# Optimization experiments

Hardware: AMD Instinct MI355X
Metric: run time of the kernel (lower is better)

The kernel has to match this reference:

```python
import jax, jax.numpy as jnp
import numpy as np

H, D_MODEL, D_AUX, D_POS = 8, 512, 256, 128
D_K, D_A, D_P = D_MODEL // H, D_AUX // H, D_POS // H  # 64, 32, 16
M1, M2, T, B = 8, 8, 1024, 8
EPS = 1e-12


def _l2norm(x):
    # F.normalize(x, p=2, dim=-1)
    return x / jnp.maximum(jnp.linalg.norm(x, axis=-1, keepdims=True), EPS)


def _tn_transform(S):
    # S: [B,H,T,T] pairwise <Q_t, K_s>. tn[a,b] = mean over diagonal window
    # t in [-min(M1,min(a,b)), min(M2,T-1-max(a,b))] of S[a+t, b+t].
    num = jnp.zeros_like(S)
    for t in range(-M1, M2 + 1):  # small fixed window (17 offsets)
        lo, hi = max(0, -t), T - max(0, t)
        num = num.at[..., lo:hi, lo:hi].add(S[..., lo + t:hi + t, lo + t:hi + t])
    idx = jnp.arange(T)
    mn = jnp.minimum(idx[:, None], idx[None, :])
    mx = jnp.maximum(idx[:, None], idx[None, :])
    cnt = (jnp.minimum(M1, mn) + jnp.minimum(M2, T - 1 - mx) + 1).astype(S.dtype)
    return num / cnt


def _forward(x, aux, pos, Wq, bq, Wk, bk, Wv, bv, Wqa, bqa, Wka, bka, Wqp, bqp, Wkp, bkp, WO, bO, w, wa, wp, graph_dep):
    g = graph_dep.astype(x.dtype)           # [D_K, D_K] binary dependency mask
    m_node = jnp.tile(g, (1, H))            # per-head SparseLinear mask [D_K, D_MODEL]
    m_out = jnp.tile(g, (H, H))             # W_O mask: graph_dependency.repeat(h, h)
    Q = _l2norm(jnp.einsum('btm,hkm->bhtk', x, Wq * m_node) + bq[None, :, None, :])
    K = _l2norm(jnp.einsum('btm,hkm->bhtk', x, Wk * m_node) + bk[None, :, None, :])
    V = jnp.einsum('btm,hkm->bhtk', x, Wv * m_node) + bv[None, :, None, :]
    tn = _tn_transform(jnp.einsum('bhtk,bhsk->bhts', Q, K))
    QA = _l2norm(jnp.einsum('bta,hca->bhtc', aux, Wqa) + bqa[None, :, None, :])
    KA = _l2norm(jnp.einsum('bta,hca->bhtc', aux, Wka) + bka[None, :, None, :])
    QP = _l2norm(jnp.einsum('btp,hcp->bhtc', pos, Wqp) + bqp[None, :, None, :])
    KP = _l2norm(jnp.einsum('btp,hcp->bhtc', pos, Wkp) + bkp[None, :, None, :])
    sim = (w[0, 0] * tn
           + wa[0, 0] * jnp.einsum('bhtc,bhsc->bhts', QA, KA)
           + wp[0, 0] * jnp.einsum('bhtc,bhsc->bhts', QP, KP))
    attn = jax.nn.softmax(sim, axis=-1)     # [B,H,T,T]
    deta = jnp.einsum('bhts,bhsk->bhtk', attn, V).transpose(0, 2, 1, 3).reshape(B, T, D_MODEL)
    out = x + jnp.einsum('btd,ed->bte', deta, WO * m_out) + bO
    attn_matrix = attn.transpose(0, 2, 1, 3).reshape(B, T, H * T)
    return out, attn_matrix, deta


def setup_inputs() -> dict:
    key = jax.random.key(0)
    ks = jax.random.split(key, 16)
    sc = 0.05
    f32 = jnp.float32
    return {
        'x': jax.random.normal(ks[0], (B, T, D_MODEL), f32),
        'aux': jax.random.normal(ks[1], (B, T, D_AUX), f32),
        'pos': jax.random.normal(ks[2], (B, T, D_POS), f32),
        'Wq': jax.random.normal(ks[3], (H, D_K, D_MODEL), f32) * sc,
        'bq': jnp.zeros((H, D_K), f32),
        'Wk': jax.random.normal(ks[4], (H, D_K, D_MODEL), f32) * sc,
        'bk': jnp.zeros((H, D_K), f32),
        'Wv': jax.random.normal(ks[5], (H, D_K, D_MODEL), f32) * sc,
        'bv': jnp.zeros((H, D_K), f32),
        'Wqa': jax.random.normal(ks[6], (H, D_A, D_AUX), f32) * sc,
        'bqa': jnp.zeros((H, D_A), f32),
        'Wka': jax.random.normal(ks[7], (H, D_A, D_AUX), f32) * sc,
        'bka': jnp.zeros((H, D_A), f32),
        'Wqp': jax.random.normal(ks[8], (H, D_P, D_POS), f32) * sc,
        'bqp': jnp.zeros((H, D_P), f32),
        'Wkp': jax.random.normal(ks[9], (H, D_P, D_POS), f32) * sc,
        'bkp': jnp.zeros((H, D_P), f32),
        'WO': jax.random.normal(ks[10], (D_MODEL, D_MODEL), f32) * sc,
        'bO': jnp.zeros((D_MODEL,), f32),
        'w': jax.random.normal(ks[11], (1, 1), f32),
        'wa': jax.random.normal(ks[12], (1, 1), f32),
        'wp': jax.random.normal(ks[13], (1, 1), f32),
        'graph_dep': jax.random.randint(ks[14], (D_K, D_K), 0, 2, jnp.int32),
    }


def reference(x, aux, pos, Wq, bq, Wk, bk, Wv, bv, Wqa, bqa, Wka, bka, Wqp, bqp, Wkp, bkp, WO, bO, w, wa, wp, graph_dep):
    return _forward(x, aux, pos, Wq, bq, Wk, bk, Wv, bv, Wqa, bqa, Wka, bka, Wqp, bqp, Wkp, bkp, WO, bO, w, wa, wp, graph_dep)
```

## Files before the change

### kernel.cpp

```cpp
#include <hip/hip_runtime.h>
#include <math.h>

#define NB 8
#define NH 8
#define NT 1024
#define DMODEL 512

typedef short bh8 __attribute__((ext_vector_type(8)));
typedef float fx4 __attribute__((ext_vector_type(4)));

__device__ __forceinline__ unsigned short f2bf(float f) {
  union { float f; unsigned int u; } v; v.f = f;
  unsigned int u = v.u + 0x7FFFu + ((v.u >> 16) & 1u);
  return (unsigned short)(u >> 16);
}
__device__ __forceinline__ float bf2f(unsigned short h) {
  union { unsigned int u; float f; } v; v.u = ((unsigned int)h) << 16;
  return v.f;
}

__global__ __launch_bounds__(256) void k_prep(
    const float* __restrict__ Wq, const float* __restrict__ Wk,
    const float* __restrict__ Wv, const float* __restrict__ WO,
    const int* __restrict__ g,
    const float* __restrict__ Wqa, const float* __restrict__ Wka,
    const float* __restrict__ Wqp, const float* __restrict__ Wkp,
    unsigned short* __restrict__ Wqkvcm, unsigned short* __restrict__ WO_mb,
    unsigned short* __restrict__ Wacm, unsigned short* __restrict__ Wpcm,
    unsigned short* __restrict__ qcf, unsigned short* __restrict__ kcf)
{
  int stride = gridDim.x * 256;
  int tid0 = blockIdx.x * 256 + threadIdx.x;
  for (int i = tid0; i < 1536 * 512; i += stride) {
    int m = i & 511;
    int j = i >> 9;
    int k = j & 63;
    int hh = (j >> 6) & 7;
    int qkv = j >> 9;
    const float* W = (qkv == 0) ? Wq : (qkv == 1 ? Wk : Wv);
    float val = W[(hh * 64 + k) * 512 + m] * (float)g[k * 64 + (m & 63)];
    Wqkvcm[((size_t)(m >> 3) * 1536 + j) * 8 + (m & 7)] = f2bf(val);
  }
  for (int i = tid0; i < 512 * 512; i += stride) {
    int d = i & 511, e = i >> 9;
    WO_mb[i] = f2bf(WO[i] * (float)g[(e & 63) * 64 + (d & 63)]);
  }
  for (int i = tid0; i < 512 * 256; i += stride) {
    int a = i & 255, j = i >> 8;
    float val = (j < 256) ? Wqa[j * 256 + a] : Wka[(j - 256) * 256 + a];
    Wacm[((size_t)(a >> 3) * 512 + j) * 8 + (a & 7)] = f2bf(val);
  }
  for (int i = tid0; i < 256 * 128; i += stride) {
    int p = i & 127, j = i >> 7;
    float val = (j < 128) ? Wqp[j * 128 + p] : Wkp[(j - 128) * 128 + p];
    Wpcm[((size_t)(p >> 3) * 256 + j) * 8 + (p & 7)] = f2bf(val);
  }
  for (int i = tid0; i < 64 * 16384; i += stride) {
    int bh = i >> 14, rest = i & 16383;
    size_t addr = (size_t)(bh * 8 + 6) * 8192 + rest;
    qcf[addr] = 0; kcf[addr] = 0;
  }
}

__global__ __launch_bounds__(256) void k_tocm(
    const float* __restrict__ src, unsigned short* __restrict__ dst, int M, int K)
{
  __shared__ unsigned short t16[64][80];
  const int bm = blockIdx.x * 64, bk = blockIdx.y * 64;
  const int tid = threadIdx.x;
  {
    int r = tid >> 2, q = tid & 3;
    const float* sp = src + (size_t)(bm + r) * K + bk + q * 16;
#pragma unroll
    for (int j = 0; j < 4; ++j) {
      float4 v = *(const float4*)(sp + j * 4);
      t16[r][q * 16 + j * 4 + 0] = f2bf(v.x);
      t16[r][q * 16 + j * 4 + 1] = f2bf(v.y);
      t16[r][q * 16 + j * 4 + 2] = f2bf(v.z);
      t16[r][q * 16 + j * 4 + 3] = f2bf(v.w);
    }
  }
  __syncthreads();
  {
    int cq = tid >> 5, rr = tid & 31;
#pragma unroll
    for (int h = 0; h < 2; ++h) {
      int r2 = rr + h * 32;
      unsigned short* dp = dst + ((size_t)((bk >> 3) + cq) * M + bm + r2) * 8;
      *(int4*)dp = *(const int4*)&t16[r2][cq * 8];
    }
  }
}

__global__ __launch_bounds__(256) void k_gqkv(
    const unsigned short* __restrict__ Acm, const unsigned short* __restrict__ Bcm,
    const float* __restrict__ bq, const float* __restrict__ bk, const float* __restrict__ bv,
    const float* __restrict__ w,
    unsigned short* __restrict__ Qf, unsigned short* __restrict__ Kf,
    unsigned short* __restrict__ Vrow)
{
  const int M = 8192, N = 1536, K = 512;
  const int bm = blockIdx.y * 128, bn = blockIdx.x * 128;
  const int tid = threadIdx.x, lane = tid & 63, wv = tid >> 6;
  const int wr = wv >> 1, wc = wv & 1;
  const int lrow = lane & 15, lgrp = lane >> 4;
  fx4 acc[4][4];
#pragma unroll
  for (int m = 0; m < 4; ++m)
#pragma unroll
    for (int n = 0; n < 4; ++n) acc[m][n] = (fx4){0.f, 0.f, 0.f, 0.f};
  for (int k0 = 0; k0 < K; k0 += 32) {
    bh8 af[4], bf[4];
#pragma unroll
    for (int m = 0; m < 4; ++m)
      af[m] = *(const bh8*)(Acm + (((size_t)((k0 >> 3) + lgrp)) * M + bm + wr * 64 + m * 16 + lrow) * 8);
#pragma unroll
    for (int n = 0; n < 4; ++n)
      bf[n] = *(const bh8*)(Bcm + (((size_t)((k0 >> 3) + lgrp)) * N + bn + wc * 64 + n * 16 + lrow) * 8);
#pragma unroll
    for (int m = 0; m < 4; ++m)
#pragma unroll
      for (int n = 0; n < 4; ++n)
        acc[m][n] = __builtin_amdgcn_mfma_f32_16x16x32_bf16(af[m], bf[n], acc[m][n], 0, 0, 0);
  }
  const int qkv = bn >> 9;
  const int hh = ((bn + wc * 64) >> 6) & 7;
  const float w0 = w[0];
  const float* bias = (qkv == 0) ? bq : (qkv == 1 ? bk : bv);
  float bvals[4];
#pragma unroll
  for (int n = 0; n < 4; ++n) bvals[n] = bias[hh * 64 + n * 16 + lrow];
#pragma unroll
  for (int m = 0; m < 4; ++m)
#pragma unroll
    for (int r = 0; r < 4; ++r) {
      int row = bm + wr * 64 + m * 16 + lgrp * 4 + r;
      int b = row >> 10, t = row & 1023;
      int bh = b * 8 + hh;
      float v0 = acc[m][0][r] + bvals[0];
      float v1 = acc[m][1][r] + bvals[1];
      float v2 = acc[m][2][r] + bvals[2];
      float v3 = acc[m][3][r] + bvals[3];
      if (qkv < 2) {
        float p = v0 * v0 + v1 * v1 + v2 * v2 + v3 * v3;
        p += __shfl_xor(p, 1); p += __shfl_xor(p, 2);
        p += __shfl_xor(p, 4); p += __shfl_xor(p, 8);
        float rn = 1.0f / fmaxf(sqrtf(p), 1e-12f);
        if (qkv == 0) rn *= w0;
        unsigned short* dst = (qkv == 0) ? Qf : Kf;
        size_t base = (size_t)bh * 65536 + (size_t)(lrow >> 3) * 8192 + (size_t)t * 8 + (lrow & 7);
        dst[base + 0 * 16384] = f2bf(v0 * rn);
        dst[base + 1 * 16384] = f2bf(v1 * rn);
        dst[base + 2 * 16384] = f2bf(v2 * rn);
        dst[base + 3 * 16384] = f2bf(v3 * rn);
      } else {
        size_t vb = ((size_t)bh * NT + t) * 64 + lrow;
        Vrow[vb + 0]  = f2bf(v0);
        Vrow[vb + 16] = f2bf(v1);
        Vrow[vb + 32] = f2bf(v2);
        Vrow[vb + 48] = f2bf(v3);
      }
    }
}

__global__ __launch_bounds__(256) void k_gaux(
    const unsigned short* __restrict__ Acm, const unsigned short* __restrict__ Bcm,
    const float* __restrict__ bqa, const float* __restrict__ bka,
    const float* __restrict__ wa,
    unsigned short* __restrict__ qcf, unsigned short* __restrict__ kcf)
{
  const int M = 8192, N = 512, K = 256;
  const int bm = blockIdx.y * 128, bn = blockIdx.x * 128;
  const int tid = threadIdx.x, lane = tid & 63, wv = tid >> 6;
  const int wr = wv >> 1, wc = wv & 1;
  const int lrow = lane & 15, lgrp = lane >> 4;
  fx4 acc[4][4];
#pragma unroll
  for (int m = 0; m < 4; ++m)
#pragma unroll
    for (int n = 0; n < 4; ++n) acc[m][n] = (fx4){0.f, 0.f, 0.f, 0.f};
  for (int k0 = 0; k0 < K; k0 += 32) {
    bh8 af[4], bf[4];
#pragma unroll
    for (int m = 0; m < 4; ++m)
      af[m] = *(const bh8*)(Acm + (((size_t)((k0 >> 3) + lgrp)) * M + bm + wr * 64 + m * 16 + lrow) * 8);
#pragma unroll
    for (int n = 0; n < 4; ++n)
      bf[n] = *(const bh8*)(Bcm + (((size_t)((k0 >> 3) + lgrp)) * N + bn + wc * 64 + n * 16 + lrow) * 8);
#pragma unroll
    for (int m = 0; m < 4; ++m)
#pragma unroll
      for (int n = 0; n < 4; ++n)
        acc[m][n] = __builtin_amdgcn_mfma_f32_16x16x32_bf16(af[m], bf[n], acc[m][n], 0, 0, 0);
  }
  const int isK = (bn >> 8) & 1;
  const int hh0 = (((bn & 255) + wc * 64) >> 5) & 7;
  const float wa0 = wa[0];
  const float* bias = isK ? bka : bqa;
  float bvals[4];
#pragma unroll
  for (int n = 0; n < 4; ++n) bvals[n] = bias[(hh0 + (n >> 1)) * 32 + (n & 1) * 16 + lrow];
  unsigned short* dst = isK ? kcf : qcf;
  const float scale = isK ? 1.0f : wa0;
#pragma unroll
  for (int m = 0; m < 4; ++m)
#pragma unroll
    for (int r = 0; r < 4; ++r) {
      int row = bm + wr * 64 + m * 16 + lgrp * 4 + r;
      int b = row >> 10, t = row & 1023;
      float v0 = acc[m][0][r] + bvals[0];
      float v1 = acc[m][1][r] + bvals[1];
      float v2 = acc[m][2][r] + bvals[2];
      float v3 = acc[m][3][r] + bvals[3];
      float plo = v0 * v0 + v1 * v1;
      float phi = v2 * v2 + v3 * v3;
      plo += __shfl_xor(plo, 1); plo += __shfl_xor(plo, 2);
      plo += __shfl_xor(plo, 4); plo += __shfl_xor(plo, 8);
      phi += __shfl_xor(phi, 1); phi += __shfl_xor(phi, 2);
      phi += __shfl_xor(phi, 4); phi += __shfl_xor(phi, 8);
      float rlo = scale / fmaxf(sqrtf(plo), 1e-12f);
      float rhi = scale / fmaxf(sqrtf(phi), 1e-12f);
      size_t b0 = (size_t)(b * 8 + hh0) * 65536 + (size_t)(lrow >> 3) * 8192 + (size_t)t * 8 + (lrow & 7);
      size_t b1 = (size_t)(b * 8 + hh0 + 1) * 65536 + (size_t)(lrow >> 3) * 8192 + (size_t)t * 8 + (lrow & 7);
      dst[b0 + 0]     = f2bf(v0 * rlo);
      dst[b0 + 16384] = f2bf(v1 * rlo);
      dst[b1 + 0]     = f2bf(v2 * rhi);
      dst[b1 + 16384] = f2bf(v3 * rhi);
    }
}

__global__ __launch_bounds__(256) void k_gpos(
    const unsigned short* __restrict__ Acm, const unsigned short* __restrict__ Bcm,
    const float* __restrict__ bqp, const float* __restrict__ bkp,
    const float* __restrict__ wp,
    unsigned short* __restrict__ qcf, unsigned short* __restrict__ kcf)
{
  const int M = 8192, N = 256, K = 128;
  const int bm = blockIdx.y * 128, bn = blockIdx.x * 128;
  const int tid = threadIdx.x, lane = tid & 63, wv = tid >> 6;
  const int wr = wv >> 1, wc = wv & 1;
  const int lrow = lane & 15, lgrp = lane >> 4;
  fx4 acc[4][4];
#pragma unroll
  for (int m = 0; m < 4; ++m)
#pragma unroll
    for (int n = 0; n < 4; ++n) acc[m][n] = (fx4){0.f, 0.f, 0.f, 0.f};
  for (int k0 = 0; k0 < K; k0 += 32) {
    bh8 af[4], bf[4];
#pragma unroll
    for (int m = 0; m < 4; ++m)
      af[m] = *(const bh8*)(Acm + (((size_t)((k0 >> 3) + lgrp)) * M + bm + wr * 64 + m * 16 + lrow) * 8);
#pragma unroll
    for (int n = 0; n < 4; ++n)
      bf[n] = *(const bh8*)(Bcm + (((size_t)((k0 >> 3) + lgrp)) * N + bn + wc * 64 + n * 16 + lrow) * 8);
#pragma unroll
    for (int m = 0; m < 4; ++m)
#pragma unroll
      for (int n = 0; n < 4; ++n)
        acc[m][n] = __builtin_amdgcn_mfma_f32_16x16x32_bf16(af[m], bf[n], acc[m][n], 0, 0, 0);
  }
  const int isK = (bn >> 7) & 1;
  const int bh0 = (((bn & 127) + wc * 64) >> 4) & 7;
  const float wp0 = wp[0];
  const float* bias = isK ? bkp : bqp;
  float bvals[4];
#pragma unroll
  for (int n = 0; n < 4; ++n) bvals[n] = bias[(bh0 + n) * 16 + lrow];
  unsigned short* dst = isK ? kcf : qcf;
  const float scale = isK ? 1.0f : wp0;
#pragma unroll
  for (int m = 0; m < 4; ++m)
#pragma unroll
    for (int r = 0; r < 4; ++r) {
      int row = bm + wr * 64 + m * 16 + lgrp * 4 + r;
      int b = row >> 10, t = row & 1023;
      float v[4];
      v[0] = acc[m][0][r] + bvals[0];
      v[1] = acc[m][1][r] + bvals[1];
      v[2] = acc[m][2][r] + bvals[2];
      v[3] = acc[m][3][r] + bvals[3];
#pragma unroll
      for (int n = 0; n < 4; ++n) {
        float p = v[n] * v[n];
        p += __shfl_xor(p, 1); p += __shfl_xor(p, 2);
        p += __shfl_xor(p, 4); p += __shfl_xor(p, 8);
        float rn = scale / fmaxf(sqrtf(p), 1e-12f);
        size_t addr = (size_t)(b * 8 + bh0 + n) * 65536 + (size_t)(4 + (lrow >> 3)) * 8192
                    + (size_t)t * 8 + (lrow & 7);
        dst[addr] = f2bf(v[n] * rn);
      }
    }
}

__global__ __launch_bounds__(256) void k_vtr(
    const unsigned short* __restrict__ Vrow, unsigned short* __restrict__ Vc)
{
  __shared__ unsigned short tile[64][72];
  const int tt = blockIdx.x, bh = blockIdx.y;
  const int tid = threadIdx.x;
  const int r = tid & 63, g = tid >> 6;
  const unsigned short* src = Vrow + ((size_t)bh * NT + tt * 64 + r) * 64 + g * 16;
  int4 v0 = *(const int4*)(src);
  int4 v1 = *(const int4*)(src + 8);
  const unsigned short* pv0 = (const unsigned short*)&v0;
  const unsigned short* pv1 = (const unsigned short*)&v1;
#pragma unroll
  for (int j = 0; j < 8; ++j) tile[g * 16 + j][r] = pv0[j];
#pragma unroll
  for (int j = 0; j < 8; ++j) tile[g * 16 + 8 + j][r] = pv1[j];
  __syncthreads();
  unsigned short* dst0 = Vc + ((size_t)(bh * 128 + tt * 8 + g * 2) * 64 + r) * 8;
  unsigned short* dst1 = Vc + ((size_t)(bh * 128 + tt * 8 + g * 2 + 1) * 64 + r) * 8;
  *(int4*)dst0 = *(const int4*)&tile[r][g * 16];
  *(int4*)dst1 = *(const int4*)&tile[r][g * 16 + 8];
}

__global__ __launch_bounds__(256) void k_sim(
    const unsigned short* __restrict__ Qf, const unsigned short* __restrict__ Kf,
    const unsigned short* __restrict__ qcf, const unsigned short* __restrict__ kcf,
    float* __restrict__ lsumP, float* __restrict__ attn)
{
  __shared__ float Se[80][81];
  __shared__ unsigned short Pd[64][66];
  const int flat = blockIdx.x;
  const int wgid = (flat & 7) * 512 + (flat >> 3);
  const int bh = wgid >> 6;
  const int ctg = (wgid >> 4) & 3;
  const int at = wgid & 15;
  const int a0 = at * 64;
  const int b = bh >> 3, hh = bh & 7;
  const int tid = threadIdx.x;
  const int lane = tid & 63, wv = tid >> 6;
  const int lrow16 = lane & 15, lgrp = lane >> 4;
  const bh8 zfrag = {0, 0, 0, 0, 0, 0, 0, 0};
  const int base_cl = (wv * 16 + lane) & 63;
  float lacc[16];
#pragma unroll
  for (int s = 0; s < 16; ++s) lacc[s] = 0.f;

  const unsigned short* Qc = Qf + (size_t)(bh * 8 + lgrp) * NT * 8;
  const unsigned short* Kc = Kf + (size_t)(bh * 8 + lgrp) * NT * 8;

  bh8 qa0, qa1;
  {
    const unsigned short* qb = qcf + ((size_t)(bh * 8 + lgrp) * NT + a0 + wv * 16 + lrow16) * 8;
    qa0 = *(const bh8*)(qb);
    qa1 = *(const bh8*)(qb + (size_t)4 * NT * 8);
  }

  for (int ct = ctg * 4; ct < ctg * 4 + 4; ++ct) {
    const int c0 = ct * 64;
    __syncthreads();

#pragma unroll
    for (int i = 0; i < 7; ++i) {
      int tt = wv + 4 * i;
      if (tt < 25) {
        int tr = tt / 5, tc = tt % 5;
        int ar = a0 - 8 + tr * 16 + lrow16;
        int kr = c0 - 8 + tc * 16 + lrow16;
        bool av = (unsigned)ar < (unsigned)NT;
        bool bv = (unsigned)kr < (unsigned)NT;
        const unsigned short* ap = Qc + (size_t)(av ? ar : 0) * 8;
        const unsigned short* bp = Kc + (size_t)(bv ? kr : 0) * 8;
        bh8 af0 = av ? *(const bh8*)(ap) : zfrag;
        bh8 af1 = av ? *(const bh8*)(ap + (size_t)4 * NT * 8) : zfrag;
        bh8 bf0 = bv ? *(const bh8*)(bp) : zfrag;
        bh8 bf1 = bv ? *(const bh8*)(bp + (size_t)4 * NT * 8) : zfrag;
        fx4 acc = {0.f, 0.f, 0.f, 0.f};
        acc = __builtin_amdgcn_mfma_f32_16x16x32_bf16(af0, bf0, acc, 0, 0, 0);
        acc = __builtin_amdgcn_mfma_f32_16x16x32_bf16(af1, bf1, acc, 0, 0, 0);
#pragma unroll
        for (int r = 0; r < 4; ++r)
          Se[tr * 16 + lgrp * 4 + r][tc * 16 + lrow16] = acc[r];
      }
    }

#pragma unroll
    for (int n = 0; n < 4; ++n) {
      const unsigned short* kb = kcf + ((size_t)(bh * 8 + lgrp) * NT + c0 + n * 16 + lrow16) * 8;
      bh8 kb0 = *(const bh8*)(kb);
      bh8 kb1 = *(const bh8*)(kb + (size_t)4 * NT * 8);
      fx4 pacc = {0.f, 0.f, 0.f, 0.f};
      pacc = __builtin_amdgcn_mfma_f32_16x16x32_bf16(qa0, kb0, pacc, 0, 0, 0);
      pacc = __builtin_amdgcn_mfma_f32_16x16x32_bf16(qa1, kb1, pacc, 0, 0, 0);
#pragma unroll
      for (int r = 0; r < 4; ++r)
        Pd[wv * 16 + lgrp * 4 + r][n * 16 + lrow16] = f2bf(pacc[r]);
    }

    __syncthreads();

    float dval = 0.f;
    {
      int rr = wv * 16 + lrow16;
#pragma unroll
      for (int u = 0; u <= 16; ++u) dval += Se[rr + u][u];
    }

    float num = 0.f;
#pragma unroll
    for (int s = 0; s < 16; ++s) {
      int a_l = wv * 16 + s;
      int c_l = (base_cl + s) & 63;
      if (s == 0) {
        num = 0.f;
#pragma unroll
        for (int u = 0; u <= 16; ++u) num += Se[a_l + u][c_l + u];
      } else {
        int cm1 = (c_l == 0) ? 0 : (c_l - 1);
        float up = Se[a_l + 16][c_l + 16] - Se[a_l - 1][cm1];
        float dS = __shfl(dval, s);
        num = (c_l == 0) ? dS : (num + up);
      }
      int a = a0 + a_l, c = c0 + c_l;
      int mn = min(a, c), mx = max(a, c);
      float cntf = (float)(min(8, mn) + min(8, 1023 - mx) + 1);
      float sim = num * __builtin_amdgcn_rcpf(cntf) + bf2f(Pd[a_l][c_l]);
      float pe = __expf(sim);
      lacc[s] += pe;
      attn[(((size_t)(b * NT + a)) * NH + hh) * NT + c] = pe;
    }
  }

#pragma unroll
  for (int s = 0; s < 16; ++s) {
    float v = lacc[s];
#pragma unroll
    for (int off = 32; off; off >>= 1) v += __shfl_xor(v, off);
    if (lane == 0)
      lsumP[(size_t)ctg * 65536 + (size_t)bh * NT + a0 + wv * 16 + s] = v;
  }
}

__global__ __launch_bounds__(256) void k_pv(
    const unsigned short* __restrict__ Vc, const float* __restrict__ lsumP,
    float* __restrict__ attn, float* __restrict__ deta,
    unsigned short* __restrict__ detab)
{
  const int at = blockIdx.x, bh = blockIdx.y;
  const int a0 = at * 64;
  const int b = bh >> 3, hh = bh & 7;
  const int tid = threadIdx.x, lane = tid & 63, wv = tid >> 6;
  const int lrow = lane & 15, lgrp = lane >> 4;
  const int arow = a0 + wv * 16 + lrow;
  const size_t lidx = (size_t)bh * NT + arow;
  const float rl = 1.0f / (lsumP[lidx] + lsumP[65536 + lidx]
                           + lsumP[131072 + lidx] + lsumP[196608 + lidx]);
  fx4 acc0 = {0.f,0.f,0.f,0.f}, acc1 = {0.f,0.f,0.f,0.f};
  fx4 acc2 = {0.f,0.f,0.f,0.f}, acc3 = {0.f,0.f,0.f,0.f};
  float* arowp = attn + (((size_t)(b * NT + arow)) * NH + hh) * NT;
  for (int ct = 0; ct < 16; ++ct) {
    const int c0 = ct * 64;
#pragma unroll
    for (int kh = 0; kh < 2; ++kh) {
      float* pp = arowp + c0 + kh * 32 + lgrp * 8;
      float4 p0 = *(float4*)pp;
      float4 p1 = *(float4*)(pp + 4);
      p0.x *= rl; p0.y *= rl; p0.z *= rl; p0.w *= rl;
      p1.x *= rl; p1.y *= rl; p1.z *= rl; p1.w *= rl;
      *(float4*)pp = p0;
      *(float4*)(pp + 4) = p1;
      bh8 af;
      unsigned short* afp = (unsigned short*)&af;
      afp[0] = f2bf(p0.x); afp[1] = f2bf(p0.y); afp[2] = f2bf(p0.z); afp[3] = f2bf(p0.w);
      afp[4] = f2bf(p1.x); afp[5] = f2bf(p1.y); afp[6] = f2bf(p1.z); afp[7] = f2bf(p1.w);
      const unsigned short* vk = Vc + ((size_t)(bh * 128 + (c0 >> 3) + kh * 4 + lgrp) * 64 + lrow) * 8;
      acc0 = __builtin_amdgcn_mfma_f32_16x16x32_bf16(af, *(const bh8*)(vk + 0 * 16 * 8), acc0, 0, 0, 0);
      acc1 = __builtin_amdgcn_mfma_f32_16x16x32_bf16(af, *(const bh8*)(vk + 1 * 16 * 8), acc1, 0, 0, 0);
      acc2 = __builtin_amdgcn_mfma_f32_16x16x32_bf16(af, *(const bh8*)(vk + 2 * 16 * 8), acc2, 0, 0, 0);
      acc3 = __builtin_amdgcn_mfma_f32_16x16x32_bf16(af, *(const bh8*)(vk + 3 * 16 * 8), acc3, 0, 0, 0);
    }
  }
  const int orow = a0 + wv * 16 + lgrp * 4;
#pragma unroll
  for (int r = 0; r < 4; ++r) {
    size_t rb = ((size_t)(b * NT + orow + r)) * DMODEL + hh * 64 + lrow;
    deta[rb + 0]  = acc0[r]; detab[rb + 0]  = f2bf(acc0[r]);
    deta[rb + 16] = acc1[r]; detab[rb + 16] = f2bf(acc1[r]);
    deta[rb + 32] = acc2[r]; detab[rb + 32] = f2bf(acc2[r]);
    deta[rb + 48] = acc3[r]; detab[rb + 48] = f2bf(acc3[r]);
  }
}

__global__ __launch_bounds__(256) void k_gout(
    const unsigned short* __restrict__ A, const unsigned short* __restrict__ B,
    float* __restrict__ C, int K, int N,
    const float* __restrict__ X, const float* __restrict__ bias)
{
  const int bm = blockIdx.y * 128, bn = blockIdx.x * 128;
  const int tid = threadIdx.x, lane = tid & 63, wv = tid >> 6;
  const int wr = wv >> 1, wc = wv & 1;
  const int lrow = lane & 15, lgrp = lane >> 4;
  fx4 acc[4][4];
#pragma unroll
  for (int m = 0; m < 4; ++m)
#pragma unroll
    for (int n = 0; n < 4; ++n) acc[m][n] = (fx4){0.f, 0.f, 0.f, 0.f};
  const unsigned short* Ab = A + (size_t)(bm + wr * 64 + lrow) * K + lgrp * 8;
  const unsigned short* Bb = B + (size_t)(bn + wc * 64 + lrow) * K + lgrp * 8;
  for (int k0 = 0; k0 < K; k0 += 32) {
    bh8 af[4], bf[4];
#pragma unroll
    for (int m = 0; m < 4; ++m) af[m] = *(const bh8*)(Ab + (size_t)m * 16 * K + k0);
#pragma unroll
    for (int n = 0; n < 4; ++n) bf[n] = *(const bh8*)(Bb + (size_t)n * 16 * K + k0);
#pragma unroll
    for (int m = 0; m < 4; ++m)
#pragma unroll
      for (int n = 0; n < 4; ++n)
        acc[m][n] = __builtin_amdgcn_mfma_f32_16x16x32_bf16(af[m], bf[n], acc[m][n], 0, 0, 0);
  }
#pragma unroll
  for (int m = 0; m < 4; ++m)
#pragma unroll
    for (int n = 0; n < 4; ++n)
#pragma unroll
      for (int r = 0; r < 4; ++r) {
        int row = bm + wr * 64 + m * 16 + lgrp * 4 + r;
        int col = bn + wc * 64 + n * 16 + lrow;
        C[(size_t)row * N + col] = acc[m][n][r] + X[(size_t)row * N + col] + bias[col];
      }
}

extern "C" void kernel_launch(void* const* d_in, const int* in_sizes, int n_in,
                              void* d_out, int out_size, void* d_ws, size_t ws_size,
                              hipStream_t stream) {
  const float* x   = (const float*)d_in[0];
  const float* aux = (const float*)d_in[1];
  const float* pos = (const float*)d_in[2];
  const float* Wq  = (const float*)d_in[3];
  const float* bq  = (const float*)d_in[4];
  const float* Wk  = (const float*)d_in[5];
  const float* bk  = (const float*)d_in[6];
  const float* Wv  = (const float*)d_in[7];
  const float* bv  = (const float*)d_in[8];
  const float* Wqa = (const float*)d_in[9];
  const float* bqa = (const float*)d_in[10];
  const float* Wka = (const float*)d_in[11];
  const float* bka = (const float*)d_in[12];
  const float* Wqp = (const float*)d_in[13];
  const float* bqp = (const float*)d_in[14];
  const float* Wkp = (const float*)d_in[15];
  const float* bkp = (const float*)d_in[16];
  const float* WO  = (const float*)d_in[17];
  const float* bO  = (const float*)d_in[18];
  const float* w   = (const float*)d_in[19];
  const float* wa  = (const float*)d_in[20];
  const float* wp  = (const float*)d_in[21];
  const int*   gdep = (const int*)d_in[22];

  float* out  = (float*)d_out;
  float* attn = out + (size_t)4194304;
  float* deta = out + (size_t)71303168;

  unsigned short* xcm   = (unsigned short*)attn;
  unsigned short* auxcm = xcm + 4194304;
  unsigned short* poscm = auxcm + 2097152;

  unsigned short* Qf = (unsigned short*)out;
  unsigned short* Kf = (unsigned short*)deta;

  float* ws = (float*)d_ws;
  float* lsumP = ws;
  unsigned short* Wqkvcm = (unsigned short*)(ws + 262144);
  unsigned short* WO_mb  = Wqkvcm + 786432;
  unsigned short* Wacm   = WO_mb + 262144;
  unsigned short* Wpcm   = Wacm + 131072;
  unsigned short* Vrow   = Wpcm + 32768;
  unsigned short* Vc     = Vrow + 4194304;
  unsigned short* qcf    = Vc + 4194304;
  unsigned short* kcf    = qcf + 4194304;
  unsigned short* detab  = kcf + 4194304;

  k_prep<<<512, 256, 0, stream>>>(Wq, Wk, Wv, WO, gdep, Wqa, Wka, Wqp, Wkp,
                                  Wqkvcm, WO_mb, Wacm, Wpcm, qcf, kcf);
  k_tocm<<<dim3(128, 8), 256, 0, stream>>>(x, xcm, 8192, 512);
  k_tocm<<<dim3(128, 4), 256, 0, stream>>>(aux, auxcm, 8192, 256);
  k_tocm<<<dim3(128, 2), 256, 0, stream>>>(pos, poscm, 8192, 128);
  k_gqkv<<<dim3(12, 64), 256, 0, stream>>>(xcm, Wqkvcm, bq, bk, bv, w, Qf, Kf, Vrow);
  k_gaux<<<dim3(4, 64), 256, 0, stream>>>(auxcm, Wacm, bqa, bka, wa, qcf, kcf);
  k_gpos<<<dim3(2, 64), 256, 0, stream>>>(poscm, Wpcm, bqp, bkp, wp, qcf, kcf);
  k_vtr<<<dim3(16, 64), 256, 0, stream>>>(Vrow, Vc);
  k_sim<<<4096, 256, 0, stream>>>(Qf, Kf, qcf, kcf, lsumP, attn);
  k_pv<<<dim3(16, 64), 256, 0, stream>>>(Vc, lsumP, attn, deta, detab);
  k_gout<<<dim3(4, 64), 256, 0, stream>>>(detab, WO_mb, out, 512, 512, x, bO);
}
```

Before: 466.7 us.

## Stage unnormalized probabilities in bf16 workspace and specialize interior tiles

k_sim now writes the unnormalized exp values as bf16 into a workspace buffer instead of fp32 into the attn output. k_pv then reads the bf16 values, writes the normalized fp32 attn once, and applies the 1/rowsum scale to the accumulated PV output. This replaces an fp32 write, read and rewrite of the large attn tensor with a bf16 write and read plus one fp32 write. Tiles away from the sequence edges use a constant 1/17 divisor instead of computing the count, and column tiles per block go from 4 to 8, halving the partial-sum slots. The bf16 path only runs when the workspace is large enough, and feeding bf16-rounded exp values into the attention output costs some accuracy.

```diff
diff --git a/kernel.cpp b/kernel.cpp
--- a/kernel.cpp
+++ b/kernel.cpp
@@ -312,20 +312,65 @@
   unsigned short* dst0 = Vc + ((size_t)(bh * 128 + tt * 8 + g * 2) * 64 + r) * 8;
   unsigned short* dst1 = Vc + ((size_t)(bh * 128 + tt * 8 + g * 2 + 1) * 64 + r) * 8;
   *(int4*)dst0 = *(const int4*)&tile[r][g * 16];
-  *(int4*)dst1 = *(const int4*)&tile[r][g * 16 + 8];
-}
-
+  *(int4*)(dst1) = *(const int4*)&tile[r][g * 16 + 8];
+}
+
+template<bool EDGE, bool PBM>
+__device__ __forceinline__ void slide_body(
+    const float (*Se)[81], const unsigned short (*Pd)[66],
+    int a0, int c0, int b, int hh, int wv, int lane, int base_cl,
+    float* lacc, float* __restrict__ attn, unsigned short* __restrict__ PB)
+{
+  float dval = 0.f;
+  {
+    int rr = wv * 16 + (lane & 15);
+#pragma unroll
+    for (int u = 0; u <= 16; ++u) dval += Se[rr + u][u];
+  }
+  float num = 0.f;
+#pragma unroll
+  for (int s = 0; s < 16; ++s) {
+    int a_l = wv * 16 + s;
+    int c_l = (base_cl + s) & 63;
+    if (s == 0) {
+      num = 0.f;
+#pragma unroll
+      for (int u = 0; u <= 16; ++u) num += Se[a_l + u][c_l + u];
+    } else {
+      int cm1 = (c_l == 0) ? 0 : (c_l - 1);
+      float up = Se[a_l + 16][c_l + 16] - Se[a_l - 1][cm1];
+      float dS = __shfl(dval, s);
+      num = (c_l == 0) ? dS : (num + up);
+    }
+    int a = a0 + a_l, c = c0 + c_l;
+    float sim;
+    if (EDGE) {
+      int mn = min(a, c), mx = max(a, c);
+      float cntf = (float)(min(8, mn) + min(8, 1023 - mx) + 1);
+      sim = num * __builtin_amdgcn_rcpf(cntf) + bf2f(Pd[a_l][c_l]);
+    } else {
+      sim = num * (1.0f / 17.0f) + bf2f(Pd[a_l][c_l]);
+    }
+    float pe = __expf(sim);
+    lacc[s] += pe;
+    size_t oidx = (((size_t)(b * NT + a)) * NH + hh) * NT + c;
+    if (PBM) PB[oidx] = f2bf(pe);
+    else     attn[oidx] = pe;
+  }
+}
+
+template<bool PBM>
 __global__ __launch_bounds__(256) void k_sim(
     const unsigned short* __restrict__ Qf, const unsigned short* __restrict__ Kf,
     const unsigned short* __restrict__ qcf, const unsigned short* __restrict__ kcf,
-    float* __restrict__ lsumP, float* __restrict__ attn)
+    float* __restrict__ lsumP, float* __restrict__ attn, unsigned short* __restrict__ PB)
 {
   __shared__ float Se[80][81];
   __shared__ unsigned short Pd[64][66];
   const int flat = blockIdx.x;
-  const int wgid = (flat & 7) * 512 + (flat >> 3);
-  const int bh = wgid >> 6;
-  const int ctg = (wgid >> 4) & 3;
+  const int wgid = (flat & 7) * 256 + (flat >> 3);
+  const int bh = wgid >> 5;
+  const int ctg = (wgid >> 4) & 1;
   const int at = wgid & 15;
   const int a0 = at * 64;
   const int b = bh >> 3, hh = bh & 7;
@@ -348,7 +393,7 @@
     qa1 = *(const bh8*)(qb + (size_t)4 * NT * 8);
   }
 
-  for (int ct = ctg * 4; ct < ctg * 4 + 4; ++ct) {
+  for (int ct = ctg * 8; ct < ctg * 8 + 8; ++ct) {
     const int c0 = ct * 64;
     __syncthreads();
 
@@ -391,36 +436,11 @@
 
     __syncthreads();
 
-    float dval = 0.f;
-    {
-      int rr = wv * 16 + lrow16;
-#pragma unroll
-      for (int u = 0; u <= 16; ++u) dval += Se[rr + u][u];
-    }
-
-    float num = 0.f;
-#pragma unroll
-    for (int s = 0; s < 16; ++s) {
-      int a_l = wv * 16 + s;
-      int c_l = (base_cl + s) & 63;
-      if (s == 0) {
-        num = 0.f;
-#pragma unroll
-        for (int u = 0; u <= 16; ++u) num += Se[a_l + u][c_l + u];
-      } else {
-        int cm1 = (c_l == 0) ? 0 : (c_l - 1);
-        float up = Se[a_l + 16][c_l + 16] - Se[a_l - 1][cm1];
-        float dS = __shfl(dval, s);
-        num = (c_l == 0) ? dS : (num + up);
-      }
-      int a = a0 + a_l, c = c0 + c_l;
-      int mn = min(a, c), mx = max(a, c);
-      float cntf = (float)(min(8, mn) + min(8, 1023 - mx) + 1);
-      float sim = num * __builtin_amdgcn_rcpf(cntf) + bf2f(Pd[a_l][c_l]);
-      float pe = __expf(sim);
-      lacc[s] += pe;
-      attn[(((size_t)(b * NT + a)) * NH + hh) * NT + c] = pe;
-    }
+    bool edge = (ct == 0) || (ct == 15) || (at == 0) || (at == 15);
+    if (edge)
+      slide_body<true, PBM>(Se, Pd, a0, c0, b, hh, wv, lane, base_cl, lacc, attn, PB);
+    else
+      slide_body<false, PBM>(Se, Pd, a0, c0, b, hh, wv, lane, base_cl, lacc, attn, PB);
   }
 
 #pragma unroll
@@ -433,10 +453,11 @@
   }
 }
 
+template<bool PBM>
 __global__ __launch_bounds__(256) void k_pv(
     const unsigned short* __restrict__ Vc, const float* __restrict__ lsumP,
-    float* __restrict__ attn, float* __restrict__ deta,
-    unsigned short* __restrict__ detab)
+    float* __restrict__ attn, const unsigned short* __restrict__ PB,
+    float* __restrict__ deta, unsigned short* __restrict__ detab)
 {
   const int at = blockIdx.x, bh = blockIdx.y;
   const int a0 = at * 64;
@@ -445,26 +466,38 @@
   const int lrow = lane & 15, lgrp = lane >> 4;
   const int arow = a0 + wv * 16 + lrow;
   const size_t lidx = (size_t)bh * NT + arow;
-  const float rl = 1.0f / (lsumP[lidx] + lsumP[65536 + lidx]
-                           + lsumP[131072 + lidx] + lsumP[196608 + lidx]);
+  const float rl = 1.0f / (lsumP[lidx] + lsumP[65536 + lidx]);
   fx4 acc0 = {0.f,0.f,0.f,0.f}, acc1 = {0.f,0.f,0.f,0.f};
   fx4 acc2 = {0.f,0.f,0.f,0.f}, acc3 = {0.f,0.f,0.f,0.f};
   float* arowp = attn + (((size_t)(b * NT + arow)) * NH + hh) * NT;
+  const unsigned short* pbrow = PBM ? (PB + (((size_t)(b * NT + arow)) * NH + hh) * NT) : nullptr;
   for (int ct = 0; ct < 16; ++ct) {
     const int c0 = ct * 64;
 #pragma unroll
     for (int kh = 0; kh < 2; ++kh) {
-      float* pp = arowp + c0 + kh * 32 + lgrp * 8;
-      float4 p0 = *(float4*)pp;
-      float4 p1 = *(float4*)(pp + 4);
-      p0.x *= rl; p0.y *= rl; p0.z *= rl; p0.w *= rl;
-      p1.x *= rl; p1.y *= rl; p1.z *= rl; p1.w *= rl;
-      *(float4*)pp = p0;
-      *(float4*)(pp + 4) = p1;
       bh8 af;
-      unsigned short* afp = (unsigned short*)&af;
-      afp[0] = f2bf(p0.x); afp[1] = f2bf(p0.y); afp[2] = f2bf(p0.z); afp[3] = f2bf(p0.w);
-      afp[4] = f2bf(p1.x); afp[5] = f2bf(p1.y); afp[6] = f2bf(p1.z); afp[7] = f2bf(p1.w);
+      if (PBM) {
+        af = *(const bh8*)(pbrow + c0 + kh * 32 + lgrp * 8);
+        const unsigned short* ap = (const unsigned short*)&af;
+        float4 o0, o1;
+        o0.x = bf2f(ap[0]) * rl; o0.y = bf2f(ap[1]) * rl;
+        o0.z = bf2f(ap[2]) * rl; o0.w = bf2f(ap[3]) * rl;
+        o1.x = bf2f(ap[4]) * rl; o1.y = bf2f(ap[5]) * rl;
+        o1.z = bf2f(ap[6]) * rl; o1.w = bf2f(ap[7]) * rl;
+        *(float4*)(arowp + c0 + kh * 32 + lgrp * 8) = o0;
+        *(float4*)(arowp + c0 + kh * 32 + lgrp * 8 + 4) = o1;
+      } else {
+        float* pp = arowp + c0 + kh * 32 + lgrp * 8;
+        float4 p0 = *(float4*)pp;
+        float4 p1 = *(float4*)(pp + 4);
+        p0.x *= rl; p0.y *= rl; p0.z *= rl; p0.w *= rl;
+        p1.x *= rl; p1.y *= rl; p1.z *= rl; p1.w *= rl;
+        *(float4*)pp = p0;
+        *(float4*)(pp + 4) = p1;
+        unsigned short* afp = (unsigned short*)&af;
+        afp[0] = f2bf(p0.x); afp[1] = f2bf(p0.y); afp[2] = f2bf(p0.z); afp[3] = f2bf(p0.w);
+        afp[4] = f2bf(p1.x); afp[5] = f2bf(p1.y); afp[6] = f2bf(p1.z); afp[7] = f2bf(p1.w);
+      }
       const unsigned short* vk = Vc + ((size_t)(bh * 128 + (c0 >> 3) + kh * 4 + lgrp) * 64 + lrow) * 8;
       acc0 = __builtin_amdgcn_mfma_f32_16x16x32_bf16(af, *(const bh8*)(vk + 0 * 16 * 8), acc0, 0, 0, 0);
       acc1 = __builtin_amdgcn_mfma_f32_16x16x32_bf16(af, *(const bh8*)(vk + 1 * 16 * 8), acc1, 0, 0, 0);
@@ -475,11 +508,17 @@
   const int orow = a0 + wv * 16 + lgrp * 4;
 #pragma unroll
   for (int r = 0; r < 4; ++r) {
+    float sc = 1.0f;
+    if (PBM) {
+      size_t li = (size_t)bh * NT + orow + r;
+      sc = 1.0f / (lsumP[li] + lsumP[65536 + li]);
+    }
     size_t rb = ((size_t)(b * NT + orow + r)) * DMODEL + hh * 64 + lrow;
-    deta[rb + 0]  = acc0[r]; detab[rb + 0]  = f2bf(acc0[r]);
-    deta[rb + 16] = acc1[r]; detab[rb + 16] = f2bf(acc1[r]);
-    deta[rb + 32] = acc2[r]; detab[rb + 32] = f2bf(acc2[r]);
-    deta[rb + 48] = acc3[r]; detab[rb + 48] = f2bf(acc3[r]);
+    float d0 = acc0[r] * sc, d1 = acc1[r] * sc, d2 = acc2[r] * sc, d3 = acc3[r] * sc;
+    deta[rb + 0]  = d0; detab[rb + 0]  = f2bf(d0);
+    deta[rb + 16] = d1; detab[rb + 16] = f2bf(d1);
+    deta[rb + 32] = d2; detab[rb + 32] = f2bf(d2);
+    deta[rb + 48] = d3; detab[rb + 48] = f2bf(d3);
   }
 }
 
@@ -563,7 +602,7 @@
 
   float* ws = (float*)d_ws;
   float* lsumP = ws;
-  unsigned short* Wqkvcm = (unsigned short*)(ws + 262144);
+  unsigned short* Wqkvcm = (unsigned short*)(ws + 131072);
   unsigned short* WO_mb  = Wqkvcm + 786432;
   unsigned short* Wacm   = WO_mb + 262144;
   unsigned short* Wpcm   = Wacm + 131072;
@@ -572,6 +611,10 @@
   unsigned short* qcf    = Vc + 4194304;
   unsigned short* kcf    = qcf + 4194304;
   unsigned short* detab  = kcf + 4194304;
+  unsigned short* PB     = detab + 4194304;
+
+  const size_t NEED_PB = 179109888ull;
+  const bool pbm = (ws_size >= NEED_PB);
 
   k_prep<<<512, 256, 0, stream>>>(Wq, Wk, Wv, WO, gdep, Wqa, Wka, Wqp, Wkp,
                                   Wqkvcm, WO_mb, Wacm, Wpcm, qcf, kcf);
@@ -582,7 +625,12 @@
   k_gaux<<<dim3(4, 64), 256, 0, stream>>>(auxcm, Wacm, bqa, bka, wa, qcf, kcf);
   k_gpos<<<dim3(2, 64), 256, 0, stream>>>(poscm, Wpcm, bqp, bkp, wp, qcf, kcf);
   k_vtr<<<dim3(16, 64), 256, 0, stream>>>(Vrow, Vc);
-  k_sim<<<4096, 256, 0, stream>>>(Qf, Kf, qcf, kcf, lsumP, attn);
-  k_pv<<<dim3(16, 64), 256, 0, stream>>>(Vc, lsumP, attn, deta, detab);
+  if (pbm) {
+    k_sim<true><<<2048, 256, 0, stream>>>(Qf, Kf, qcf, kcf, lsumP, attn, PB);
+    k_pv<true><<<dim3(16, 64), 256, 0, stream>>>(Vc, lsumP, attn, PB, deta, detab);
+  } else {
+    k_sim<false><<<2048, 256, 0, stream>>>(Qf, Kf, qcf, kcf, lsumP, attn, PB);
+    k_pv<false><<<dim3(16, 64), 256, 0, stream>>>(Vc, lsumP, attn, PB, deta, detab);
+  }
   k_gout<<<dim3(4, 64), 256, 0, stream>>>(detab, WO_mb, out, 512, 512, x, bO);
 }
```

Measured after the change: 403.5 us, median of 2. 13.6% less time.

## Fuse similarity and PV into one kernel with bf16 probability scratch

Applied to the files above, without the earlier changes.

Merges the softmax-numerator kernel and the PV kernel. Each workgroup now walks all 16 column tiles for its 64 rows, keeps the exponentiated scores in shared memory and accumulates P·V with MFMA in the same loop. Unnormalized probabilities go to a bf16 scratch buffer and are rescaled into the fp32 attention output at the end, replacing the earlier fp32 write, read and rewrite of the whole attention matrix. Interior tiles use a constant 1/17 divisor instead of computing per-element window counts. The trade-offs are that attention weights and deta are now rounded through bf16, launch parallelism drops to 1024 workgroups, and a large extra workspace region plus a small bf16-to-fp32 deta conversion kernel are needed.

```diff
diff --git a/kernel.cpp b/kernel.cpp
--- a/kernel.cpp
+++ b/kernel.cpp
@@ -312,20 +312,66 @@
   unsigned short* dst0 = Vc + ((size_t)(bh * 128 + tt * 8 + g * 2) * 64 + r) * 8;
   unsigned short* dst1 = Vc + ((size_t)(bh * 128 + tt * 8 + g * 2 + 1) * 64 + r) * 8;
   *(int4*)dst0 = *(const int4*)&tile[r][g * 16];
-  *(int4*)dst1 = *(const int4*)&tile[r][g * 16 + 8];
-}
-
-__global__ __launch_bounds__(256) void k_sim(
+  *(int4*)(dst1) = *(const int4*)&tile[r][g * 16 + 8];
+}
+
+template<bool EDGE>
+__device__ __forceinline__ void slide_body(
+    const float (*Se)[81], unsigned short (*Pd)[72],
+    int a0, int c0, int b, int hh, int wv, int lane, int base_cl,
+    float* lacc, unsigned short* __restrict__ PB)
+{
+  float dval = 0.f;
+  {
+    int rr = wv * 16 + (lane & 15);
+#pragma unroll
+    for (int u = 0; u <= 16; ++u) dval += Se[rr + u][u];
+  }
+  float num = 0.f;
+#pragma unroll
+  for (int s = 0; s < 16; ++s) {
+    int a_l = wv * 16 + s;
+    int c_l = (base_cl + s) & 63;
+    if (s == 0) {
+      num = 0.f;
+#pragma unroll
+      for (int u = 0; u <= 16; ++u) num += Se[a_l + u][c_l + u];
+    } else {
+      int cm1 = (c_l == 0) ? 0 : (c_l - 1);
+      float up = Se[a_l + 16][c_l + 16] - Se[a_l - 1][cm1];
+      float dS = __shfl(dval, s);
+      num = (c_l == 0) ? dS : (num + up);
+    }
+    int a = a0 + a_l, c = c0 + c_l;
+    float sim;
+    if (EDGE) {
+      int mn = min(a, c), mx = max(a, c);
+      float cntf = (float)(min(8, mn) + min(8, 1023 - mx) + 1);
+      sim = num * __builtin_amdgcn_rcpf(cntf) + bf2f(Pd[a_l][c_l]);
+    } else {
+      sim = num * (1.0f / 17.0f) + bf2f(Pd[a_l][c_l]);
+    }
+    float pe = __expf(sim);
+    lacc[s] += pe;
+    unsigned short peb = f2bf(pe);
+    Pd[a_l][c_l] = peb;
+    PB[(((size_t)(b * NT + a)) * NH + hh) * NT + c] = peb;
+  }
+}
+
+__global__ __launch_bounds__(256) void k_simpv(
     const unsigned short* __restrict__ Qf, const unsigned short* __restrict__ Kf,
     const unsigned short* __restrict__ qcf, const unsigned short* __restrict__ kcf,
-    float* __restrict__ lsumP, float* __restrict__ attn)
+    const unsigned short* __restrict__ Vc,
+    unsigned short* __restrict__ PB, float* __restrict__ attn,
+    unsigned short* __restrict__ detab)
 {
   __shared__ float Se[80][81];
-  __shared__ unsigned short Pd[64][66];
+  __shared__ unsigned short Pd[64][72];
+  __shared__ float rsum[64];
   const int flat = blockIdx.x;
-  const int wgid = (flat & 7) * 512 + (flat >> 3);
-  const int bh = wgid >> 6;
-  const int ctg = (wgid >> 4) & 3;
+  const int wgid = (flat & 7) * 128 + (flat >> 3);
+  const int bh = wgid >> 4;
   const int at = wgid & 15;
   const int a0 = at * 64;
   const int b = bh >> 3, hh = bh & 7;
@@ -337,6 +383,9 @@
   float lacc[16];
 #pragma unroll
   for (int s = 0; s < 16; ++s) lacc[s] = 0.f;
+  fx4 oacc[4];
+#pragma unroll
+  for (int n = 0; n < 4; ++n) oacc[n] = (fx4){0.f, 0.f, 0.f, 0.f};
 
   const unsigned short* Qc = Qf + (size_t)(bh * 8 + lgrp) * NT * 8;
   const unsigned short* Kc = Kf + (size_t)(bh * 8 + lgrp) * NT * 8;
@@ -348,7 +397,7 @@
     qa1 = *(const bh8*)(qb + (size_t)4 * NT * 8);
   }
 
-  for (int ct = ctg * 4; ct < ctg * 4 + 4; ++ct) {
+  for (int ct = 0; ct < 16; ++ct) {
     const int c0 = ct * 64;
     __syncthreads();
 
@@ -391,35 +440,20 @@
 
     __syncthreads();
 
-    float dval = 0.f;
-    {
-      int rr = wv * 16 + lrow16;
-#pragma unroll
-      for (int u = 0; u <= 16; ++u) dval += Se[rr + u][u];
-    }
-
-    float num = 0.f;
-#pragma unroll
-    for (int s = 0; s < 16; ++s) {
-      int a_l = wv * 16 + s;
-      int c_l = (base_cl + s) & 63;
-      if (s == 0) {
-        num = 0.f;
-#pragma unroll
-        for (int u = 0; u <= 16; ++u) num += Se[a_l + u][c_l + u];
-      } else {
-        int cm1 = (c_l == 0) ? 0 : (c_l - 1);
-        float up = Se[a_l + 16][c_l + 16] - Se[a_l - 1][cm1];
-        float dS = __shfl(dval, s);
-        num = (c_l == 0) ? dS : (num + up);
-      }
-      int a = a0 + a_l, c = c0 + c_l;
-      int mn = min(a, c), mx = max(a, c);
-      float cntf = (float)(min(8, mn) + min(8, 1023 - mx) + 1);
-      float sim = num * __builtin_amdgcn_rcpf(cntf) + bf2f(Pd[a_l][c_l]);
-      float pe = __expf(sim);
-      lacc[s] += pe;
-      attn[(((size_t)(b * NT + a)) * NH + hh) * NT + c] = pe;
+    bool edge = (ct == 0) || (ct == 15) || (at == 0) || (at == 15);
+    if (edge)
+      slide_body<true>(Se, Pd, a0, c0, b, hh, wv, lane, base_cl, lacc, PB);
+    else
+      slide_body<false>(Se, Pd, a0, c0, b, hh, wv, lane, base_cl, lacc, PB);
+
+#pragma unroll
+    for (int kh = 0; kh < 2; ++kh) {
+      bh8 pf = *(const bh8*)&Pd[wv * 16 + lrow16][kh * 32 + lgrp * 8];
+      const unsigned short* vk = Vc + ((size_t)(bh * 128 + ct * 8 + kh * 4 + lgrp) * 64 + lrow16) * 8;
+      oacc[0] = __builtin_amdgcn_mfma_f32_16x16x32_bf16(pf, *(const bh8*)(vk + 0 * 16 * 8), oacc[0], 0, 0, 0);
+      oacc[1] = __builtin_amdgcn_mfma_f32_16x16x32_bf16(pf, *(const bh8*)(vk + 1 * 16 * 8), oacc[1], 0, 0, 0);
+      oacc[2] = __builtin_amdgcn_mfma_f32_16x16x32_bf16(pf, *(const bh8*)(vk + 2 * 16 * 8), oacc[2], 0, 0, 0);
+      oacc[3] = __builtin_amdgcn_mfma_f32_16x16x32_bf16(pf, *(const bh8*)(vk + 3 * 16 * 8), oacc[3], 0, 0, 0);
     }
   }
 
@@ -428,59 +462,56 @@
     float v = lacc[s];
 #pragma unroll
     for (int off = 32; off; off >>= 1) v += __shfl_xor(v, off);
-    if (lane == 0)
-      lsumP[(size_t)ctg * 65536 + (size_t)bh * NT + a0 + wv * 16 + s] = v;
-  }
-}
-
-__global__ __launch_bounds__(256) void k_pv(
-    const unsigned short* __restrict__ Vc, const float* __restrict__ lsumP,
-    float* __restrict__ attn, float* __restrict__ deta,
-    unsigned short* __restrict__ detab)
-{
-  const int at = blockIdx.x, bh = blockIdx.y;
-  const int a0 = at * 64;
-  const int b = bh >> 3, hh = bh & 7;
-  const int tid = threadIdx.x, lane = tid & 63, wv = tid >> 6;
-  const int lrow = lane & 15, lgrp = lane >> 4;
-  const int arow = a0 + wv * 16 + lrow;
-  const size_t lidx = (size_t)bh * NT + arow;
-  const float rl = 1.0f / (lsumP[lidx] + lsumP[65536 + lidx]
-                           + lsumP[131072 + lidx] + lsumP[196608 + lidx]);
-  fx4 acc0 = {0.f,0.f,0.f,0.f}, acc1 = {0.f,0.f,0.f,0.f};
-  fx4 acc2 = {0.f,0.f,0.f,0.f}, acc3 = {0.f,0.f,0.f,0.f};
-  float* arowp = attn + (((size_t)(b * NT + arow)) * NH + hh) * NT;
-  for (int ct = 0; ct < 16; ++ct) {
-    const int c0 = ct * 64;
-#pragma unroll
-    for (int kh = 0; kh < 2; ++kh) {
-      float* pp = arowp + c0 + kh * 32 + lgrp * 8;
-      float4 p0 = *(float4*)pp;
-      float4 p1 = *(float4*)(pp + 4);
-      p0.x *= rl; p0.y *= rl; p0.z *= rl; p0.w *= rl;
-      p1.x *= rl; p1.y *= rl; p1.z *= rl; p1.w *= rl;
-      *(float4*)pp = p0;
-      *(float4*)(pp + 4) = p1;
-      bh8 af;
-      unsigned short* afp = (unsigned short*)&af;
-      afp[0] = f2bf(p0.x); afp[1] = f2bf(p0.y); afp[2] = f2bf(p0.z); afp[3] = f2bf(p0.w);
-      afp[4] = f2bf(p1.x); afp[5] = f2bf(p1.y); afp[6] = f2bf(p1.z); afp[7] = f2bf(p1.w);
-      const unsigned short* vk = Vc + ((size_t)(bh * 128 + (c0 >> 3) + kh * 4 + lgrp) * 64 + lrow) * 8;
-      acc0 = __builtin_amdgcn_mfma_f32_16x16x32_bf16(af, *(const bh8*)(vk + 0 * 16 * 8), acc0, 0, 0, 0);
-      acc1 = __builtin_amdgcn_mfma_f32_16x16x32_bf16(af, *(const bh8*)(vk + 1 * 16 * 8), acc1, 0, 0, 0);
-      acc2 = __builtin_amdgcn_mfma_f32_16x16x32_bf16(af, *(const bh8*)(vk + 2 * 16 * 8), acc2, 0, 0, 0);
-      acc3 = __builtin_amdgcn_mfma_f32_16x16x32_bf16(af, *(const bh8*)(vk + 3 * 16 * 8), acc3, 0, 0, 0);
-    }
-  }
+    if (lane == 0) rsum[wv * 16 + s] = v;
+  }
+
   const int orow = a0 + wv * 16 + lgrp * 4;
 #pragma unroll
   for (int r = 0; r < 4; ++r) {
-    size_t rb = ((size_t)(b * NT + orow + r)) * DMODEL + hh * 64 + lrow;
-    deta[rb + 0]  = acc0[r]; detab[rb + 0]  = f2bf(acc0[r]);
-    deta[rb + 16] = acc1[r]; detab[rb + 16] = f2bf(acc1[r]);
-    deta[rb + 32] = acc2[r]; detab[rb + 32] = f2bf(acc2[r]);
-    deta[rb + 48] = acc3[r]; detab[rb + 48] = f2bf(acc3[r]);
-  }
+    float sc = 1.0f / rsum[wv * 16 + lgrp * 4 + r];
+    size_t rb = ((size_t)(b * NT + orow + r)) * DMODEL + hh * 64 + lrow16;
+    detab[rb + 0]  = f2bf(oacc[0][r] * sc);
+    detab[rb + 16] = f2bf(oacc[1][r] * sc);
+    detab[rb + 32] = f2bf(oacc[2][r] * sc);
+    detab[rb + 48] = f2bf(oacc[3][r] * sc);
+  }
+
+  __syncthreads();
+
+  {
+    const int rowl = tid >> 2;
+    const int colq = tid & 3;
+    const float rlv = 1.0f / rsum[rowl];
+    const size_t rbase = (((size_t)(b * NT + a0 + rowl)) * NH + hh) * NT;
+    const unsigned short* pbr = PB + rbase;
+    float* atr = attn + rbase;
+#pragma unroll 4
+    for (int cc = 0; cc < 32; ++cc) {
+      int col = colq * 8 + cc * 32;
+      bh8 p8 = *(const bh8*)(pbr + col);
+      const unsigned short* pp = (const unsigned short*)&p8;
+      float4 o0, o1;
+      o0.x = bf2f(pp[0]) * rlv; o0.y = bf2f(pp[1]) * rlv;
+      o0.z = bf2f(pp[2]) * rlv; o0.w = bf2f(pp[3]) * rlv;
+      o1.x = bf2f(pp[4]) * rlv; o1.y = bf2f(pp[5]) * rlv;
+      o1.z = bf2f(pp[6]) * rlv; o1.w = bf2f(pp[7]) * rlv;
+      *(float4*)(atr + col) = o0;
+      *(float4*)(atr + col + 4) = o1;
+    }
+  }
+}
+
+__global__ __launch_bounds__(256) void k_deta(
+    const unsigned short* __restrict__ detab, float* __restrict__ deta)
+{
+  int i = blockIdx.x * 256 + threadIdx.x;
+  bh8 v = *(const bh8*)(detab + (size_t)i * 8);
+  const unsigned short* p = (const unsigned short*)&v;
+  float4 o0, o1;
+  o0.x = bf2f(p[0]); o0.y = bf2f(p[1]); o0.z = bf2f(p[2]); o0.w = bf2f(p[3]);
+  o1.x = bf2f(p[4]); o1.y = bf2f(p[5]); o1.z = bf2f(p[6]); o1.w = bf2f(p[7]);
+  *(float4*)(deta + (size_t)i * 8) = o0;
+  *(float4*)(deta + (size_t)i * 8 + 4) = o1;
 }
 
 __global__ __launch_bounds__(256) void k_gout(
@@ -561,9 +592,7 @@
   unsigned short* Qf = (unsigned short*)out;
   unsigned short* Kf = (unsigned short*)deta;
 
-  float* ws = (float*)d_ws;
-  float* lsumP = ws;
-  unsigned short* Wqkvcm = (unsigned short*)(ws + 262144);
+  unsigned short* Wqkvcm = (unsigned short*)d_ws;
   unsigned short* WO_mb  = Wqkvcm + 786432;
   unsigned short* Wacm   = WO_mb + 262144;
   unsigned short* Wpcm   = Wacm + 131072;
@@ -572,6 +601,7 @@
   unsigned short* qcf    = Vc + 4194304;
   unsigned short* kcf    = qcf + 4194304;
   unsigned short* detab  = kcf + 4194304;
+  unsigned short* PB     = detab + 4194304;
 
   k_prep<<<512, 256, 0, stream>>>(Wq, Wk, Wv, WO, gdep, Wqa, Wka, Wqp, Wkp,
                                   Wqkvcm, WO_mb, Wacm, Wpcm, qcf, kcf);
@@ -582,7 +612,7 @@
   k_gaux<<<dim3(4, 64), 256, 0, stream>>>(auxcm, Wacm, bqa, bka, wa, qcf, kcf);
   k_gpos<<<dim3(2, 64), 256, 0, stream>>>(poscm, Wpcm, bqp, bkp, wp, qcf, kcf);
   k_vtr<<<dim3(16, 64), 256, 0, stream>>>(Vrow, Vc);
-  k_sim<<<4096, 256, 0, stream>>>(Qf, Kf, qcf, kcf, lsumP, attn);
-  k_pv<<<dim3(16, 64), 256, 0, stream>>>(Vc, lsumP, attn, deta, detab);
+  k_simpv<<<1024, 256, 0, stream>>>(Qf, Kf, qcf, kcf, Vc, PB, attn, detab);
+  k_deta<<<2048, 256, 0, stream>>>(detab, deta);
   k_gout<<<dim3(4, 64), 256, 0, stream>>>(detab, WO_mb, out, 512, 512, x, bO);
 }
```

Result: slower. 492.1 us (+5.4%).
